# Performance work log

Hardware: AMD Instinct MI355X
Metric: run time of the kernel (lower is better)

## Reference

```python
import jax, jax.numpy as jnp
import numpy as np

N_OUT = 4096
N_IN = 4096
FRAC_SPARSE = 0.5
N_SPARSE = int(FRAC_SPARSE * N_OUT * N_IN)  # 8388608
TOKENS = 256


def setup_inputs() -> dict:
    key = jax.random.key(0)
    k1, k2 = jax.random.split(key)
    # x: activations fed to F.linear
    x = jax.random.normal(k1, (TOKENS, N_IN), dtype=jnp.float32)
    # sparse_values: nn.Parameter of size n_sparse
    sparse_values = jax.random.normal(k2, (N_SPARSE,), dtype=jnp.float32) * 0.02
    # sparse_mask as sorted unique row-major flat indices of True entries.
    # torch `out[mask] = values` fills values into True positions in row-major
    # order, which equals scattering values at the ascending-sorted flat idxs.
    rng = np.random.default_rng(0)
    flat_idx = np.sort(rng.permutation(N_OUT * N_IN)[:N_SPARSE]).astype(np.int32)
    return {"x": x, "sparse_values": sparse_values, "flat_idx": jnp.asarray(flat_idx)}


def reference(x, sparse_values, flat_idx):
    # reconstruct(): dense [n_out, n_in] weight via scatter of sparse values
    W = (
        jnp.zeros((N_OUT * N_IN,), dtype=sparse_values.dtype)
        .at[flat_idx]
        .set(sparse_values)
        .reshape(N_OUT, N_IN)
    )
    # F.linear(x, W) == x @ W.T
    return x @ W.T
```

## Files before the change

### kernel.cpp

```cpp
#include <hip/hip_runtime.h>
#include <stdint.h>

#define N_OUT    4096
#define N_IN     4096
#define TOKENS   256
#define N_SPARSE 8388608
#define SPLITK   4
#define KCHUNK   256
#define NCHUNK   4
#define NSEG     (N_IN / KCHUNK)
#define CPW      (NSEG + 1)
#define BN       64
#define ADV      192

typedef __attribute__((ext_vector_type(8))) short bf16x8;
typedef __attribute__((ext_vector_type(8))) unsigned short u16x8;
typedef __attribute__((ext_vector_type(4))) float f32x4;

__device__ __forceinline__ unsigned short f2bf(float f) {
    union { float f; unsigned u; } v; v.f = f;
    unsigned r = v.u + 0x7fffu + ((v.u >> 16) & 1u);
    return (unsigned short)(r >> 16);
}

__device__ __forceinline__ float bf2f(unsigned short u) {
    union { unsigned u; float f; } v; v.u = ((unsigned)u) << 16;
    return v.f;
}

__device__ __forceinline__ void ld4(const int* __restrict__ idx,
                                    const float* __restrict__ vals,
                                    int jb, int4& i4, float4& v4) {
    if (jb + 4 <= N_SPARSE) {
        i4 = *(const int4*)(idx + jb);
        v4 = *(const float4*)(vals + jb);
    } else {
        i4 = int4{0, 0, 0, 0}; v4 = float4{0.f, 0.f, 0.f, 0.f};
        #pragma unroll
        for (int e = 0; e < 4; ++e) {
            const int j = jb + e;
            if (j < N_SPARSE) { (&i4.x)[e] = idx[j]; (&v4.x)[e] = vals[j]; }
        }
    }
}

__device__ __forceinline__ void consume4(const int4& i4, const float4& v4, int jb,
                                         int start, int end, int base,
                                         unsigned short* __restrict__ brow, int rx) {
    #pragma unroll
    for (int e = 0; e < 4; ++e) {
        const int j = jb + e;
        if (j >= start && j < end) {
            const int cc = (&i4.x)[e] - base;
            brow[((cc & ~7) ^ rx) | (cc & 7)] = f2bf((&v4.x)[e]);
        }
    }
}

__global__ void prep(const float* __restrict__ x, const int* __restrict__ idx,
                     unsigned short* __restrict__ xs, int* __restrict__ cp) {
    const int b = blockIdx.x;
    const int t = threadIdx.x;
    if (b < 1024) {
        const int i = (b * 256 + t) * 4;
        const int m = i >> 12;
        const int k = i & 4095;
        const float4 v = *(const float4*)(x + i);
        ushort4 o;
        o.x = f2bf(v.x); o.y = f2bf(v.y); o.z = f2bf(v.z); o.w = f2bf(v.w);
        const int lane = (m & 15) | (((k >> 3) & 3) << 4);
        const int addr = ((k >> 5) * 16 + (m >> 4)) * 512 + lane * 8 + (k & 7);
        *(ushort4*)(xs + addr) = o;
    } else {
        const int e = (b - 1024) * 256 + t;
        const int r = e / CPW;
        const int z = e - r * CPW;
        const int target = r * N_IN + z * KCHUNK;
        const int c = target >> 1;
        int lo = c > 16384 ? c - 16384 : 0;
        int hi = c + 16384 < N_SPARSE ? c + 16384 : N_SPARSE;
        while (lo < hi) {
            const int m = (lo + hi) >> 1;
            if (idx[m] < target) lo = m + 1; else hi = m;
        }
        cp[e] = lo;
    }
}

__global__ __launch_bounds__(512, 2) void fused_gemm(
        const unsigned short* __restrict__ xs,
        const int* __restrict__ idx,
        const float* __restrict__ vals,
        const int* __restrict__ cp,
        unsigned short* __restrict__ part)
{
    __shared__ short Bs[2][BN * KCHUNK];

    const int tid = threadIdx.x;
    const int l   = tid & 63;
    const int w   = tid >> 6;
    const int bn  = blockIdx.x;
    const int bz  = blockIdx.y;

    const int rl    = tid >> 3;
    const int sub8  = tid & 7;
    const int rglob = bn * BN + rl;
    const int rx    = (rl & 7) << 3;

    const int seg0 = bz * NCHUNK;
    int eb[NCHUNK + 1];
    #pragma unroll
    for (int q = 0; q <= NCHUNK; ++q) eb[q] = cp[rglob * CPW + seg0 + q];

    int gstart, gend, gbase, jstart;
    unsigned short* brow;
    int  bj0, bj1, bj2, bj3, bj4, bj5;
    int4 bi0, bi1, bi2, bi3, bi4, bi5;
    float4 bv0, bv1, bv2, bv3, bv4, bv5;

#define PRO(q) do { bj##q = jstart + q * 32; \
                    if (bj##q < gend) ld4(idx, vals, bj##q, bi##q, bv##q); } while (0)
#define STEP(q) do { if (bj##q < gend) { \
                        consume4(bi##q, bv##q, bj##q, gstart, gend, gbase, brow, rx); \
                        bj##q += ADV; \
                        if (bj##q < gend) ld4(idx, vals, bj##q, bi##q, bv##q); } } while (0)
#define PRO_ALL()  do { PRO(0); PRO(1); PRO(2); PRO(3); PRO(4); PRO(5); } while (0)
#define CONSUME()  while (bj0 < gend) { STEP(0); STEP(1); STEP(2); STEP(3); STEP(4); STEP(5); }
#define ZERO(nb)   do { const u16x8 z8 = {}; \
                        unsigned short* b0 = (unsigned short*)&Bs[nb][0] + tid * 32; \
                        *(u16x8*)(b0)      = z8; *(u16x8*)(b0 + 8)  = z8;  \
                        *(u16x8*)(b0 + 16) = z8; *(u16x8*)(b0 + 24) = z8; } while (0)

    gstart = eb[0]; gend = eb[1];
    gbase  = rglob * N_IN + seg0 * KCHUNK;
    jstart = (gstart & ~3) + sub8 * 4;
    brow   = (unsigned short*)&Bs[0][0] + rl * KCHUNK;
    PRO_ALL();
    ZERO(0);
    __syncthreads();
    CONSUME();
    __syncthreads();

    const int lr  = l & 15;
    const int lkg = l >> 4;
    f32x4 acc[2][4] = {};

    #pragma unroll
    for (int t = 0; t < NCHUNK; ++t) {
        const int cur = t & 1;

        if (t + 1 < NCHUNK) {
            gstart = eb[t + 1]; gend = eb[t + 2];
            gbase  = rglob * N_IN + (seg0 + t + 1) * KCHUNK;
            jstart = (gstart & ~3) + sub8 * 4;
            brow   = (unsigned short*)&Bs[cur ^ 1][0] + rl * KCHUNK;
            PRO_ALL();
            ZERO(cur ^ 1);
        }
        {
            const unsigned short* ax = xs + (size_t)((seg0 + t) * 8 * 16) * 512 + l * 8;
            const short* bsc = &Bs[cur][0];
            #pragma unroll 2
            for (int kk = 0; kk < KCHUNK / 32; ++kk) {
                bf16x8 af[2], bfr[4];
                #pragma unroll
                for (int i = 0; i < 2; ++i)
                    af[i] = *(const bf16x8*)(ax + (size_t)(kk * 16 + w * 2 + i) * 512);
                #pragma unroll
                for (int i = 0; i < 4; ++i) {
                    const int n    = i * 16 + lr;
                    const int slot = (kk * 4 + lkg) ^ (n & 7);
                    bfr[i] = *(const bf16x8*)&bsc[n * KCHUNK + slot * 8];
                }
                #pragma unroll
                for (int mi = 0; mi < 2; ++mi)
                    #pragma unroll
                    for (int ni = 0; ni < 4; ++ni)
                        acc[mi][ni] = __builtin_amdgcn_mfma_f32_16x16x32_bf16(
                                          af[mi], bfr[ni], acc[mi][ni], 0, 0, 0);
            }
        }
        __syncthreads();

        if (t + 1 < NCHUNK) {
            CONSUME();
            __syncthreads();
        }
    }
#undef PRO
#undef STEP
#undef PRO_ALL
#undef CONSUME
#undef ZERO

    unsigned short* po = part + (size_t)bz * (TOKENS * N_OUT) + (size_t)bn * BN;
    #pragma unroll
    for (int mi = 0; mi < 2; ++mi)
        #pragma unroll
        for (int r = 0; r < 4; ++r) {
            const int m = w * 32 + mi * 16 + lkg * 4 + r;
            #pragma unroll
            for (int ni = 0; ni < 4; ++ni) {
                const int n = ni * 16 + lr;
                po[(size_t)m * N_OUT + n] = f2bf(acc[mi][ni][r]);
            }
        }
}

__global__ void reduce_k(const unsigned short* __restrict__ part, float* __restrict__ out) {
    const int i = (blockIdx.x * 256 + threadIdx.x) * 8;
    float a[8] = {};
    for (int z = 0; z < SPLITK; ++z) {
        const u16x8 p = *(const u16x8*)(part + (size_t)z * (TOKENS * N_OUT) + i);
        #pragma unroll
        for (int j = 0; j < 8; ++j) a[j] += bf2f((unsigned short)p[j]);
    }
    float4 o0 = { a[0], a[1], a[2], a[3] };
    float4 o1 = { a[4], a[5], a[6], a[7] };
    *(float4*)(out + i)     = o0;
    *(float4*)(out + i + 4) = o1;
}

__global__ void fallback_rowcsr(const float* __restrict__ x, const float* __restrict__ vals,
                                const int* __restrict__ idx, float* __restrict__ out) {
    const int o = blockIdx.x;
    const int t = threadIdx.x;
    __shared__ int   scol[256];
    __shared__ float sval[256];

    int lo = 0, hi = N_SPARSE;
    const int target = o * N_IN;
    while (lo < hi) { int m = (lo + hi) >> 1; if (idx[m] < target) lo = m + 1; else hi = m; }
    const int start = lo;
    hi = N_SPARSE;
    const int target2 = target + N_IN;
    while (lo < hi) { int m = (lo + hi) >> 1; if (idx[m] < target2) lo = m + 1; else hi = m; }
    const int end = lo;

    float acc = 0.f;
    const float* xr = x + (size_t)t * N_IN;
    for (int base = start; base < end; base += 256) {
        const int k = base + t;
        if (k < end) { scol[t] = idx[k] - target; sval[t] = vals[k]; }
        __syncthreads();
        const int cnt = min(256, end - base);
        for (int j = 0; j < cnt; ++j) acc += sval[j] * xr[scol[j]];
        __syncthreads();
    }
    out[(size_t)t * N_OUT + o] = acc;
}

extern "C" void kernel_launch(void* const* d_in, const int* in_sizes, int n_in,
                              void* d_out, int out_size, void* d_ws, size_t ws_size,
                              hipStream_t stream) {
    const float* x    = (const float*)d_in[0];
    const float* vals = (const float*)d_in[1];
    const int*   idx  = (const int*)d_in[2];
    float* out = (float*)d_out;

    const size_t part_bytes = (size_t)SPLITK * TOKENS * N_OUT * 2;
    const size_t xs_bytes   = (size_t)TOKENS * N_IN * 2;
    const size_t cp_bytes   = (size_t)N_OUT * CPW * 4;
    const size_t need = part_bytes + xs_bytes + cp_bytes;

    if (ws_size >= need) {
        unsigned short* part = (unsigned short*)d_ws;
        unsigned short* xs   = (unsigned short*)((char*)d_ws + part_bytes);
        int*            cp   = (int*)((char*)d_ws + part_bytes + xs_bytes);

        prep<<<1024 + (N_OUT * CPW) / 256, 256, 0, stream>>>(x, idx, xs, cp);
        dim3 grid(N_OUT / BN, SPLITK);
        fused_gemm<<<grid, 512, 0, stream>>>(xs, idx, vals, cp, part);
        reduce_k<<<(TOKENS * N_OUT) / 2048, 256, 0, stream>>>(part, out);
    } else {
        fallback_rowcsr<<<N_OUT, TOKENS, 0, stream>>>(x, vals, idx, out);
    }
}
```

Measured before the change: 48.38 us.

## Triple-buffer sparse scatter with two-chunk-ahead loads and preloaded A fragments

```diff
diff --git a/kernel.cpp b/kernel.cpp
--- a/kernel.cpp
+++ b/kernel.cpp
@@ -11,7 +11,7 @@
 #define NSEG     (N_IN / KCHUNK)
 #define CPW      (NSEG + 1)
 #define BN       64
-#define ADV      192
+#define ADV      160
 
 typedef __attribute__((ext_vector_type(8))) short bf16x8;
 typedef __attribute__((ext_vector_type(8))) unsigned short u16x8;
@@ -87,14 +87,14 @@
     }
 }
 
-__global__ __launch_bounds__(512, 2) void fused_gemm(
+__global__ __launch_bounds__(512) void fused_gemm(
         const unsigned short* __restrict__ xs,
         const int* __restrict__ idx,
         const float* __restrict__ vals,
         const int* __restrict__ cp,
         unsigned short* __restrict__ part)
 {
-    __shared__ short Bs[2][BN * KCHUNK];
+    __shared__ short Bs[3][BN * KCHUNK];
 
     const int tid = threadIdx.x;
     const int l   = tid & 63;
@@ -106,39 +106,48 @@
     const int sub8  = tid & 7;
     const int rglob = bn * BN + rl;
     const int rx    = (rl & 7) << 3;
+    const int rowoff = rl * KCHUNK;
 
     const int seg0 = bz * NCHUNK;
     int eb[NCHUNK + 1];
     #pragma unroll
     for (int q = 0; q <= NCHUNK; ++q) eb[q] = cp[rglob * CPW + seg0 + q];
 
-    int gstart, gend, gbase, jstart;
-    unsigned short* brow;
-    int  bj0, bj1, bj2, bj3, bj4, bj5;
-    int4 bi0, bi1, bi2, bi3, bi4, bi5;
-    float4 bv0, bv1, bv2, bv3, bv4, bv5;
-
-#define PRO(q) do { bj##q = jstart + q * 32; \
-                    if (bj##q < gend) ld4(idx, vals, bj##q, bi##q, bv##q); } while (0)
-#define STEP(q) do { if (bj##q < gend) { \
-                        consume4(bi##q, bv##q, bj##q, gstart, gend, gbase, brow, rx); \
-                        bj##q += ADV; \
-                        if (bj##q < gend) ld4(idx, vals, bj##q, bi##q, bv##q); } } while (0)
-#define PRO_ALL()  do { PRO(0); PRO(1); PRO(2); PRO(3); PRO(4); PRO(5); } while (0)
-#define CONSUME()  while (bj0 < gend) { STEP(0); STEP(1); STEP(2); STEP(3); STEP(4); STEP(5); }
-#define ZERO(nb)   do { const u16x8 z8 = {}; \
-                        unsigned short* b0 = (unsigned short*)&Bs[nb][0] + tid * 32; \
-                        *(u16x8*)(b0)      = z8; *(u16x8*)(b0 + 8)  = z8;  \
-                        *(u16x8*)(b0 + 16) = z8; *(u16x8*)(b0 + 24) = z8; } while (0)
-
-    gstart = eb[0]; gend = eb[1];
-    gbase  = rglob * N_IN + seg0 * KCHUNK;
-    jstart = (gstart & ~3) + sub8 * 4;
-    brow   = (unsigned short*)&Bs[0][0] + rl * KCHUNK;
-    PRO_ALL();
+    int gsA, geA, gbA, bjA0, bjA1, bjA2, bjA3, bjA4;
+    int gsB, geB, gbB, bjB0, bjB1, bjB2, bjB3, bjB4;
+    int4 iA0, iA1, iA2, iA3, iA4, iB0, iB1, iB2, iB3, iB4;
+    float4 vA0, vA1, vA2, vA3, vA4, vB0, vB1, vB2, vB3, vB4;
+    unsigned short *browA, *browB;
+
+#define ISSUE(S, c) do { \
+        gs##S = eb[c]; ge##S = eb[(c) + 1]; \
+        gb##S = rglob * N_IN + (seg0 + (c)) * KCHUNK; \
+        brow##S = (unsigned short*)&Bs[(c) % 3][0] + rowoff; \
+        const int js = (gs##S & ~3) + sub8 * 4; \
+        bj##S##0 = js;       if (bj##S##0 < ge##S) ld4(idx, vals, bj##S##0, i##S##0, v##S##0); \
+        bj##S##1 = js + 32;  if (bj##S##1 < ge##S) ld4(idx, vals, bj##S##1, i##S##1, v##S##1); \
+        bj##S##2 = js + 64;  if (bj##S##2 < ge##S) ld4(idx, vals, bj##S##2, i##S##2, v##S##2); \
+        bj##S##3 = js + 96;  if (bj##S##3 < ge##S) ld4(idx, vals, bj##S##3, i##S##3, v##S##3); \
+        bj##S##4 = js + 128; if (bj##S##4 < ge##S) ld4(idx, vals, bj##S##4, i##S##4, v##S##4); \
+    } while (0)
+#define STEP(S, q) do { if (bj##S##q < ge##S) { \
+        consume4(i##S##q, v##S##q, bj##S##q, gs##S, ge##S, gb##S, brow##S, rx); \
+        bj##S##q += ADV; \
+        if (bj##S##q < ge##S) ld4(idx, vals, bj##S##q, i##S##q, v##S##q); } } while (0)
+#define CONSUME(S) while (bj##S##0 < ge##S || bj##S##1 < ge##S || bj##S##2 < ge##S \
+                          || bj##S##3 < ge##S || bj##S##4 < ge##S) \
+                   { STEP(S, 0); STEP(S, 1); STEP(S, 2); STEP(S, 3); STEP(S, 4); }
+#define ZERO(nb) do { const u16x8 z8 = {}; \
+        unsigned short* b0 = (unsigned short*)&Bs[nb][0] + tid * 32; \
+        *(u16x8*)(b0)      = z8; *(u16x8*)(b0 + 8)  = z8;  \
+        *(u16x8*)(b0 + 16) = z8; *(u16x8*)(b0 + 24) = z8; } while (0)
+
+    ISSUE(A, 0);
+    ISSUE(B, 1);
     ZERO(0);
+    ZERO(1);
     __syncthreads();
-    CONSUME();
+    CONSUME(A);
     __syncthreads();
 
     const int lr  = l & 15;
@@ -147,25 +156,22 @@
 
     #pragma unroll
     for (int t = 0; t < NCHUNK; ++t) {
-        const int cur = t & 1;
-
-        if (t + 1 < NCHUNK) {
-            gstart = eb[t + 1]; gend = eb[t + 2];
-            gbase  = rglob * N_IN + (seg0 + t + 1) * KCHUNK;
-            jstart = (gstart & ~3) + sub8 * 4;
-            brow   = (unsigned short*)&Bs[cur ^ 1][0] + rl * KCHUNK;
-            PRO_ALL();
-            ZERO(cur ^ 1);
-        }
+        bf16x8 afr[16];
         {
-            const unsigned short* ax = xs + (size_t)((seg0 + t) * 8 * 16) * 512 + l * 8;
-            const short* bsc = &Bs[cur][0];
-            #pragma unroll 2
+            const unsigned short* ax = xs + (size_t)((seg0 + t) * 128) * 512 + l * 8;
+            #pragma unroll
+            for (int q = 0; q < 16; ++q)
+                afr[q] = *(const bf16x8*)(ax + (size_t)((q >> 1) * 16 + w * 2 + (q & 1)) * 512);
+        }
+        if (t + 2 < NCHUNK) {
+            if (((t + 2) & 1) == 0) ISSUE(A, t + 2); else ISSUE(B, t + 2);
+            ZERO((t + 2) % 3);
+        }
+        {
+            const short* bsc = &Bs[t % 3][0];
+            #pragma unroll
             for (int kk = 0; kk < KCHUNK / 32; ++kk) {
-                bf16x8 af[2], bfr[4];
-                #pragma unroll
-                for (int i = 0; i < 2; ++i)
-                    af[i] = *(const bf16x8*)(ax + (size_t)(kk * 16 + w * 2 + i) * 512);
+                bf16x8 bfr[4];
                 #pragma unroll
                 for (int i = 0; i < 4; ++i) {
                     const int n    = i * 16 + lr;
@@ -177,19 +183,18 @@
                     #pragma unroll
                     for (int ni = 0; ni < 4; ++ni)
                         acc[mi][ni] = __builtin_amdgcn_mfma_f32_16x16x32_bf16(
-                                          af[mi], bfr[ni], acc[mi][ni], 0, 0, 0);
+                                          afr[kk * 2 + mi], bfr[ni], acc[mi][ni], 0, 0, 0);
             }
         }
         __syncthreads();
 
         if (t + 1 < NCHUNK) {
-            CONSUME();
+            if (((t + 1) & 1) == 0) { CONSUME(A); } else { CONSUME(B); }
             __syncthreads();
         }
     }
-#undef PRO
+#undef ISSUE
 #undef STEP
-#undef PRO_ALL
 #undef CONSUME
 #undef ZERO
 
```

Result: faster. 46.76 us (-3.4%).
